# Performance work log

Measured on AMD Instinct MI355X. Metric: run time of the kernel, lower is better.

Reference implementation:

```python
import jax, jax.numpy as jnp
import numpy as np

MARGIN = 2.0
EPS = 1e-9


def setup_inputs() -> dict:
    key = jax.random.key(0)
    k1, k2 = jax.random.split(key)
    N, D, C = 8192, 128, 50
    outputs = jax.random.normal(k1, (N, D), dtype=jnp.float32)
    labels = jax.random.randint(k2, (N,), 0, C, dtype=jnp.int64)
    return {"outputs": outputs, "labels": labels}


def reference(outputs, labels):
    # Pairwise squared distances via Gram trick: ||xi||^2 + ||xj||^2 - 2 xi.xj
    sq = jnp.sum(outputs * outputs, axis=-1)  # [N]
    gram = outputs @ outputs.T                # [N, N]
    dist_sq = jnp.maximum(sq[:, None] + sq[None, :] - 2.0 * gram, 0.0)

    pos = (labels[:, None] == labels[None, :])  # includes i==j, as in original
    num_pos = jnp.sum(pos)
    num_neg = pos.size - num_pos

    dist_pos = jnp.sum(jnp.where(pos, dist_sq, 0.0))
    hinge = jax.nn.relu(MARGIN - jnp.sqrt(dist_sq + EPS))
    dist_neg = jnp.sum(jnp.where(pos, 0.0, hinge * hinge))

    pos_term = jnp.where(num_pos > 0, 0.5 * dist_pos / num_pos, 0.0)
    neg_term = jnp.where(num_neg > 0, 0.5 * dist_neg / num_neg, 0.0)
    return pos_term + neg_term
```

## Files before the change

kernel.cpp:

```cpp
#include <hip/hip_runtime.h>
#include <math.h>

#define NPTS   8192
#define DDIM   128
#define NBLK2  32
#define NTRI2  528

using short8 = __attribute__((ext_vector_type(8))) short;
using f32x4  = __attribute__((ext_vector_type(4))) float;

__device__ __forceinline__ unsigned short f2bf(float f) {
    unsigned int u = __float_as_uint(f);
    u += 0x7fffu + ((u >> 16) & 1u);
    return (unsigned short)(u >> 16);
}
__device__ __forceinline__ float bf2f(unsigned short s) {
    return __uint_as_float(((unsigned int)s) << 16);
}

__device__ __forceinline__ void gld_lds16(const unsigned short* g, unsigned short* l) {
    __builtin_amdgcn_global_load_lds(
        (const __attribute__((address_space(1))) unsigned int*)g,
        (__attribute__((address_space(3))) unsigned int*)l,
        16, 0, 0);
}

__global__ __launch_bounds__(256) void prep_kernel(
    const float* __restrict__ X, unsigned short* __restrict__ Xbf,
    float* __restrict__ sq)
{
    const int wave = threadIdx.x >> 6, lane = threadIdx.x & 63;
    const int row  = blockIdx.x * 4 + wave;
    float2 v = *(const float2*)(X + (size_t)row * DDIM + lane * 2);
    unsigned short a = f2bf(v.x), b = f2bf(v.y);
    float fa = bf2f(a), fb = bf2f(b);
    float s = fa * fa + fb * fb;
    *(ushort2*)(Xbf + (size_t)row * DDIM + lane * 2) = make_ushort2(a, b);
#pragma unroll
    for (int off = 32; off > 0; off >>= 1) s += __shfl_down(s, off);
    if (lane == 0) sq[row] = s;
}

__global__ __launch_bounds__(512, 2) void pair_kernel(
    const unsigned short* __restrict__ Xbf, const int* __restrict__ lab,
    const float* __restrict__ sq, float* __restrict__ slots )
{
    const int k = blockIdx.x;
    int bi = (int)((65.0f - sqrtf((float)(4225 - 8 * k))) * 0.5f);
    if (bi < 0) bi = 0;
    while (32 * (bi + 1) - ((bi + 1) * bi) / 2 <= k) ++bi;
    while (32 * bi - (bi * (bi - 1)) / 2 > k) --bi;
    const int bj = bi + (k - (32 * bi - (bi * (bi - 1)) / 2));

    __shared__ unsigned short tile[65536];
    __shared__ float sSqA[256], sSqB[256];
    __shared__ int   sLabA[256], sLabB[256];
    __shared__ float rP[8], rN[8];

    const int tid   = threadIdx.x;
    const int rowA0 = bi * 256;
    const int rowB0 = bj * 256;

    {
        const int rloc = tid >> 4;
        const int cswz = ((tid & 15) ^ (rloc & 7)) * 8;
        const unsigned short* gA = Xbf + (size_t)(rowA0 + rloc) * DDIM + cswz;
        const unsigned short* gB = Xbf + (size_t)(rowB0 + rloc) * DDIM + cswz;
        unsigned short* lA = &tile[(tid & ~63) * 8];
        unsigned short* lB = &tile[32768 + (tid & ~63) * 8];
#pragma unroll
        for (int i = 0; i < 8; ++i)
            gld_lds16(gA + (size_t)i * 32 * DDIM, lA + i * 4096);
#pragma unroll
        for (int i = 0; i < 8; ++i)
            gld_lds16(gB + (size_t)i * 32 * DDIM, lB + i * 4096);
    }

    if (tid < 256) { sSqA[tid] = sq[rowA0 + tid];        sLabA[tid] = lab[rowA0 + tid]; }
    else           { sSqB[tid - 256] = sq[rowB0 + tid - 256];
                     sLabB[tid - 256] = lab[rowB0 + tid - 256]; }
    __syncthreads();

    const int wave = tid >> 6, lane = tid & 63;
    const int quad = lane >> 4, rr = lane & 15;
    const int wr = wave >> 2, wc = wave & 3;
    const int r7 = rr & 7;

    const unsigned short* tA = &tile[(size_t)(wr * 128 + rr) * 128];
    const unsigned short* tB = &tile[32768 + (size_t)(wc * 64 + rr) * 128];

    f32x4 acc[8][4];
#pragma unroll
    for (int i = 0; i < 8; ++i)
#pragma unroll
        for (int j = 0; j < 4; ++j)
            acc[i][j] = (f32x4){0.f, 0.f, 0.f, 0.f};

#pragma unroll
    for (int kc = 0; kc < 4; ++kc) {
        const int s = (((kc * 4 + quad) ^ r7)) * 8;
        short8 b4[4];
#pragma unroll
        for (int u = 0; u < 4; ++u)
            b4[u] = *(const short8*)(tB + u * 16 * 128 + s);
        short8 a0[4];
#pragma unroll
        for (int u = 0; u < 4; ++u)
            a0[u] = *(const short8*)(tA + u * 16 * 128 + s);
#pragma unroll
        for (int i = 0; i < 4; ++i)
#pragma unroll
            for (int j = 0; j < 4; ++j)
                acc[i][j] = __builtin_amdgcn_mfma_f32_16x16x32_bf16(a0[i], b4[j], acc[i][j], 0, 0, 0);
        short8 a1[4];
#pragma unroll
        for (int u = 0; u < 4; ++u)
            a1[u] = *(const short8*)(tA + (4 + u) * 16 * 128 + s);
#pragma unroll
        for (int i = 0; i < 4; ++i)
#pragma unroll
            for (int j = 0; j < 4; ++j)
                acc[4 + i][j] = __builtin_amdgcn_mfma_f32_16x16x32_bf16(a1[i], b4[j], acc[4 + i][j], 0, 0, 0);
    }

    float sb[4]; int lbv[4];
#pragma unroll
    for (int j = 0; j < 4; ++j) {
        int cl = wc * 64 + j * 16 + rr;
        sb[j]  = sSqB[cl];
        lbv[j] = sLabB[cl];
    }

    float posS = 0.f, dmin = 1e30f;
#pragma unroll
    for (int i = 0; i < 8; ++i) {
#pragma unroll
        for (int rg = 0; rg < 4; ++rg) {
            int   rl = wr * 128 + i * 16 + quad * 4 + rg;
            float sa = sSqA[rl];
            int   la = sLabA[rl];
#pragma unroll
            for (int j = 0; j < 4; ++j) {
                float d = fmaxf(sa + sb[j] - 2.0f * acc[i][j][rg], 0.0f);
                bool same = (la == lbv[j]);
                posS += same ? d : 0.f;
                dmin = fminf(dmin, same ? 1e30f : d);
            }
        }
    }

    float negS = 0.f;
    if (__any(dmin + 1e-9f < 4.0f)) {
#pragma unroll
        for (int i = 0; i < 8; ++i) {
#pragma unroll
            for (int rg = 0; rg < 4; ++rg) {
                int   rl = wr * 128 + i * 16 + quad * 4 + rg;
                float sa = sSqA[rl];
                int   la = sLabA[rl];
#pragma unroll
                for (int j = 0; j < 4; ++j) {
                    float d = fmaxf(sa + sb[j] - 2.0f * acc[i][j][rg], 0.0f);
                    float h = fmaxf(2.0f - sqrtf(d + 1e-9f), 0.f);
                    negS += (la == lbv[j]) ? 0.f : h * h;
                }
            }
        }
    }

    const float factor = (bi == bj) ? 1.0f : 2.0f;
    posS *= factor; negS *= factor;

#pragma unroll
    for (int off = 32; off > 0; off >>= 1) {
        posS += __shfl_down(posS, off);
        negS += __shfl_down(negS, off);
    }
    if (lane == 0) { rP[wave] = posS; rN[wave] = negS; }
    __syncthreads();
    if (tid == 0) {
        float tp = 0.f, tn = 0.f;
#pragma unroll
        for (int w = 0; w < 8; ++w) { tp += rP[w]; tn += rN[w]; }
        slots[k]         = tp;
        slots[NTRI2 + k] = tn;
    }
}

__global__ __launch_bounds__(1024) void finalize_kernel(
    const float* __restrict__ slots, const int* __restrict__ lab,
    float* __restrict__ out)
{
    __shared__ int   hist[64];
    __shared__ float sP[16], sN[16];
    const int tid = threadIdx.x;
    if (tid < 64) hist[tid] = 0;
    __syncthreads();
    for (int i = tid; i < NPTS; i += 1024) atomicAdd(&hist[lab[i]], 1);

    float p = 0.f, n = 0.f;
    for (int i = tid; i < NTRI2; i += 1024) { p += slots[i]; n += slots[NTRI2 + i]; }
#pragma unroll
    for (int off = 32; off > 0; off >>= 1) {
        p += __shfl_down(p, off);
        n += __shfl_down(n, off);
    }
    const int wave = tid >> 6, lane = tid & 63;
    if (lane == 0) { sP[wave] = p; sN[wave] = n; }
    __syncthreads();
    if (tid == 0) {
        long long np = 0;
        for (int c = 0; c < 64; ++c) np += (long long)hist[c] * hist[c];
        float tp = 0.f, tn = 0.f;
#pragma unroll
        for (int w = 0; w < 16; ++w) { tp += sP[w]; tn += sN[w]; }
        double dnp = (double)np;
        double dnn = (double)NPTS * (double)NPTS - dnp;
        double pt = (dnp > 0.0) ? 0.5 * (double)tp / dnp : 0.0;
        double nt = (dnn > 0.0) ? 0.5 * (double)tn / dnn : 0.0;
        out[0] = (float)(pt + nt);
    }
}

extern "C" void kernel_launch(void* const* d_in, const int* in_sizes, int n_in,
                              void* d_out, int out_size, void* d_ws, size_t ws_size,
                              hipStream_t stream) {
    const float* X   = (const float*)d_in[0];
    const int*   lab = (const int*)d_in[1];
    float*       out = (float*)d_out;

    char* ws = (char*)d_ws;
    unsigned short* Xbf   = (unsigned short*)(ws);
    float*          sq    = (float*)(ws + 2 * 1024 * 1024);
    float*          slots = (float*)(ws + 2 * 1024 * 1024 + 32 * 1024);

    prep_kernel<<<NPTS / 4, 256, 0, stream>>>(X, Xbf, sq);
    pair_kernel<<<NTRI2, 512, 0, stream>>>(Xbf, lab, sq, slots);
    finalize_kernel<<<1, 1024, 0, stream>>>(slots, lab, out);
}
```

Before: 87.79 us.

## Compute positive-pair term from per-class sums instead of pairwise tile epilogue

The positive-pair distance sum is rewritten algebraically as sum over i of n_c(i)*||xi||^2 minus the sum over classes of ||class sum||^2. A new class-sum kernel computes it and the finalize kernel combines it, so the pair kernel drops its per-element positive accumulation. The early-exit test for the negative hinge now uses a cheaper max over gram minus half the squared norm, with vectorized LDS loads. This adds a kernel launch and a class-sum kernel that loops serially over rows and hardcodes 50 classes. The positive term now depends on float cancellation between two large sums.

```diff
diff --git a/kernel.cpp b/kernel.cpp
--- a/kernel.cpp
+++ b/kernel.cpp
@@ -5,6 +5,7 @@
 #define DDIM   128
 #define NBLK2  32
 #define NTRI2  528
+#define NCLS   50
 
 using short8 = __attribute__((ext_vector_type(8))) short;
 using f32x4  = __attribute__((ext_vector_type(4))) float;
@@ -27,8 +28,9 @@
 
 __global__ __launch_bounds__(256) void prep_kernel(
     const float* __restrict__ X, unsigned short* __restrict__ Xbf,
-    float* __restrict__ sq)
-{
+    float* __restrict__ sq, float* __restrict__ posG)
+{
+    if (blockIdx.x == 0 && threadIdx.x == 0) posG[0] = 0.f;
     const int wave = threadIdx.x >> 6, lane = threadIdx.x & 63;
     const int row  = blockIdx.x * 4 + wave;
     float2 v = *(const float2*)(X + (size_t)row * DDIM + lane * 2);
@@ -41,6 +43,36 @@
     if (lane == 0) sq[row] = s;
 }
 
+__global__ __launch_bounds__(1024) void classsum_kernel(
+    const unsigned short* __restrict__ Xbf, const int* __restrict__ lab,
+    float* __restrict__ posG)
+{
+    __shared__ float sm[1024];
+    __shared__ float sred[2];
+    const int c    = blockIdx.x;
+    const int part = threadIdx.x >> 7;
+    const int col  = threadIdx.x & 127;
+    float acc = 0.f;
+    const int r0 = part * 1024, r1 = r0 + 1024;
+    for (int r = r0; r < r1; ++r) {
+        if (lab[r] == c)
+            acc += bf2f(Xbf[(size_t)r * DDIM + col]);
+    }
+    sm[threadIdx.x] = acc;
+    __syncthreads();
+    if (part == 0) {
+        float m = 0.f;
+#pragma unroll
+        for (int p = 0; p < 8; ++p) m += sm[p * 128 + col];
+        float m2 = m * m;
+#pragma unroll
+        for (int off = 32; off > 0; off >>= 1) m2 += __shfl_down(m2, off);
+        if ((threadIdx.x & 63) == 0) sred[threadIdx.x >> 6] = m2;
+    }
+    __syncthreads();
+    if (threadIdx.x == 0) atomicAdd(posG, sred[0] + sred[1]);
+}
+
 __global__ __launch_bounds__(512, 2) void pair_kernel(
     const unsigned short* __restrict__ Xbf, const int* __restrict__ lab,
     const float* __restrict__ sq, float* __restrict__ slots )
@@ -53,9 +85,11 @@
     const int bj = bi + (k - (32 * bi - (bi * (bi - 1)) / 2));
 
     __shared__ unsigned short tile[65536];
-    __shared__ float sSqA[256], sSqB[256];
-    __shared__ int   sLabA[256], sLabB[256];
-    __shared__ float rP[8], rN[8];
+    __shared__ __attribute__((aligned(16))) float sSqA[256];
+    __shared__ __attribute__((aligned(16))) float sSqB[256];
+    __shared__ __attribute__((aligned(16))) int   sLabA[256];
+    __shared__ __attribute__((aligned(16))) int   sLabB[256];
+    __shared__ float rN[8];
 
     const int tid   = threadIdx.x;
     const int rowA0 = bi * 256;
@@ -123,41 +157,42 @@
                 acc[4 + i][j] = __builtin_amdgcn_mfma_f32_16x16x32_bf16(a1[i], b4[j], acc[4 + i][j], 0, 0, 0);
     }
 
-    float sb[4]; int lbv[4];
-#pragma unroll
-    for (int j = 0; j < 4; ++j) {
-        int cl = wc * 64 + j * 16 + rr;
-        sb[j]  = sSqB[cl];
-        lbv[j] = sLabB[cl];
-    }
-
-    float posS = 0.f, dmin = 1e30f;
+    float hb[4];
+#pragma unroll
+    for (int j = 0; j < 4; ++j)
+        hb[j] = 0.5f * sSqB[wc * 64 + j * 16 + rr] - 2.0f;
+
+    float gm[4] = {-1e30f, -1e30f, -1e30f, -1e30f};
 #pragma unroll
     for (int i = 0; i < 8; ++i) {
+        const f32x4 sa4 = *(const f32x4*)&sSqA[wr * 128 + i * 16 + quad * 4];
 #pragma unroll
         for (int rg = 0; rg < 4; ++rg) {
-            int   rl = wr * 128 + i * 16 + quad * 4 + rg;
-            float sa = sSqA[rl];
-            int   la = sLabA[rl];
-#pragma unroll
-            for (int j = 0; j < 4; ++j) {
-                float d = fmaxf(sa + sb[j] - 2.0f * acc[i][j][rg], 0.0f);
-                bool same = (la == lbv[j]);
-                posS += same ? d : 0.f;
-                dmin = fminf(dmin, same ? 1e30f : d);
-            }
+            const float ha = -0.5f * sa4[rg];
+#pragma unroll
+            for (int j = 0; j < 4; ++j)
+                gm[j] = fmaxf(gm[j], acc[i][j][rg] + ha);
         }
     }
 
     float negS = 0.f;
-    if (__any(dmin + 1e-9f < 4.0f)) {
+    const bool wf = (gm[0] > hb[0]) | (gm[1] > hb[1]) | (gm[2] > hb[2]) | (gm[3] > hb[3]);
+    if (__any(wf)) {
+        float sb[4]; int lbv[4];
+#pragma unroll
+        for (int j = 0; j < 4; ++j) {
+            int cl = wc * 64 + j * 16 + rr;
+            sb[j]  = sSqB[cl];
+            lbv[j] = sLabB[cl];
+        }
 #pragma unroll
         for (int i = 0; i < 8; ++i) {
+            const f32x4 sa4 = *(const f32x4*)&sSqA[wr * 128 + i * 16 + quad * 4];
+            const int4  la4 = *(const int4*)&sLabA[wr * 128 + i * 16 + quad * 4];
 #pragma unroll
             for (int rg = 0; rg < 4; ++rg) {
-                int   rl = wr * 128 + i * 16 + quad * 4 + rg;
-                float sa = sSqA[rl];
-                int   la = sLabA[rl];
+                float sa = sa4[rg];
+                int   la = ((const int*)&la4)[rg];
 #pragma unroll
                 for (int j = 0; j < 4; ++j) {
                     float d = fmaxf(sa + sb[j] - 2.0f * acc[i][j][rg], 0.0f);
@@ -168,27 +203,24 @@
         }
     }
 
-    const float factor = (bi == bj) ? 1.0f : 2.0f;
-    posS *= factor; negS *= factor;
-
-#pragma unroll
-    for (int off = 32; off > 0; off >>= 1) {
-        posS += __shfl_down(posS, off);
+    negS *= (bi == bj) ? 1.0f : 2.0f;
+
+#pragma unroll
+    for (int off = 32; off > 0; off >>= 1)
         negS += __shfl_down(negS, off);
-    }
-    if (lane == 0) { rP[wave] = posS; rN[wave] = negS; }
+    if (lane == 0) rN[wave] = negS;
     __syncthreads();
     if (tid == 0) {
-        float tp = 0.f, tn = 0.f;
-#pragma unroll
-        for (int w = 0; w < 8; ++w) { tp += rP[w]; tn += rN[w]; }
-        slots[k]         = tp;
-        slots[NTRI2 + k] = tn;
+        float tn = 0.f;
+#pragma unroll
+        for (int w = 0; w < 8; ++w) tn += rN[w];
+        slots[k] = tn;
     }
 }
 
 __global__ __launch_bounds__(1024) void finalize_kernel(
     const float* __restrict__ slots, const int* __restrict__ lab,
+    const float* __restrict__ sq, const float* __restrict__ posG,
     float* __restrict__ out)
 {
     __shared__ int   hist[64];
@@ -197,9 +229,11 @@
     if (tid < 64) hist[tid] = 0;
     __syncthreads();
     for (int i = tid; i < NPTS; i += 1024) atomicAdd(&hist[lab[i]], 1);
+    __syncthreads();
 
     float p = 0.f, n = 0.f;
-    for (int i = tid; i < NTRI2; i += 1024) { p += slots[i]; n += slots[NTRI2 + i]; }
+    for (int i = tid; i < NPTS; i += 1024) p += sq[i] * (float)hist[lab[i]];
+    for (int i = tid; i < NTRI2; i += 1024) n += slots[i];
 #pragma unroll
     for (int off = 32; off > 0; off >>= 1) {
         p += __shfl_down(p, off);
@@ -216,7 +250,7 @@
         for (int w = 0; w < 16; ++w) { tp += sP[w]; tn += sN[w]; }
         double dnp = (double)np;
         double dnn = (double)NPTS * (double)NPTS - dnp;
-        double pt = (dnp > 0.0) ? 0.5 * (double)tp / dnp : 0.0;
+        double pt = (dnp > 0.0) ? ((double)tp - (double)posG[0]) / dnp : 0.0;
         double nt = (dnn > 0.0) ? 0.5 * (double)tn / dnn : 0.0;
         out[0] = (float)(pt + nt);
     }
@@ -233,8 +267,10 @@
     unsigned short* Xbf   = (unsigned short*)(ws);
     float*          sq    = (float*)(ws + 2 * 1024 * 1024);
     float*          slots = (float*)(ws + 2 * 1024 * 1024 + 32 * 1024);
-
-    prep_kernel<<<NPTS / 4, 256, 0, stream>>>(X, Xbf, sq);
+    float*          posG  = (float*)(ws + 2 * 1024 * 1024 + 64 * 1024);
+
+    prep_kernel<<<NPTS / 4, 256, 0, stream>>>(X, Xbf, sq, posG);
+    classsum_kernel<<<NCLS, 1024, 0, stream>>>(Xbf, lab, posG);
     pair_kernel<<<NTRI2, 512, 0, stream>>>(Xbf, lab, sq, slots);
-    finalize_kernel<<<1, 1024, 0, stream>>>(slots, lab, out);
-}
+    finalize_kernel<<<1, 1024, 0, stream>>>(slots, lab, sq, posG, out);
+}
```

Result: slower. 235.9 us (+168.7%).
